# Optimization experiments

Hardware: AMD Instinct MI355X
Metric: run time of the kernel (lower is better)

## Reference

```python
import jax, jax.numpy as jnp
import numpy as np

EPS = 1e-5
NEIGHBOR_K = 3
NEG_SLOPE = 0.2

def _conv(x, w):
    # x: [N,C,H,W], w: [O,I,3,3], stride 1, SAME padding
    return jax.lax.conv_general_dilated(
        x, w, window_strides=(1, 1), padding='SAME',
        dimension_numbers=('NCHW', 'OIHW', 'NCHW'))

def _bn(x, gamma, beta):
    # BatchNorm2d in training mode: batch statistics over (N,H,W), biased var
    m = x.mean(axis=(0, 2, 3), keepdims=True)
    v = x.var(axis=(0, 2, 3), keepdims=True)
    xn = (x - m) * jax.lax.rsqrt(v + EPS)
    return xn * gamma.reshape(1, -1, 1, 1) + beta.reshape(1, -1, 1, 1)

def _lrelu(x):
    return jnp.where(x >= 0, x, NEG_SLOPE * x)

def _maxpool2(x):
    return jax.lax.reduce_window(x, -jnp.inf, jax.lax.max,
                                 (1, 1, 2, 2), (1, 1, 2, 2), 'VALID')

def _features(x, w1, g1, b1, w2, g2, b2, w3, g3, b3, w4, g4, b4):
    x = _maxpool2(_lrelu(_bn(_conv(x, w1), g1, b1)))
    x = _maxpool2(_lrelu(_bn(_conv(x, w2), g2, b2)))
    x = _lrelu(_bn(_conv(x, w3), g3, b3))
    x = _lrelu(_bn(_conv(x, w4), g4, b4))
    return x  # [N, 64, 21, 21]

def setup_inputs() -> dict:
    key = jax.random.key(0)
    ks = jax.random.split(key, 8)
    inp = {
        'input1': jax.random.normal(ks[0], (32, 3, 84, 84), jnp.float32),
        'input2': jax.random.normal(ks[1], (5, 5, 3, 84, 84), jnp.float32),
        'w1': jax.random.normal(ks[2], (64, 3, 3, 3), jnp.float32) * 0.1,
        'g1': jax.random.uniform(ks[3], (64,), jnp.float32, 0.5, 1.5),
        'b1': jnp.zeros((64,), jnp.float32),
        'w2': jax.random.normal(ks[4], (64, 64, 3, 3), jnp.float32) * 0.1,
        'g2': jax.random.uniform(ks[5], (64,), jnp.float32, 0.5, 1.5),
        'b2': jnp.zeros((64,), jnp.float32),
        'w3': jax.random.normal(ks[6], (64, 64, 3, 3), jnp.float32) * 0.1,
        'g3': jax.random.uniform(ks[7], (64,), jnp.float32, 0.5, 1.5),
        'b3': jnp.zeros((64,), jnp.float32),
        'w4': jax.random.normal(jax.random.fold_in(key, 100), (64, 64, 3, 3), jnp.float32) * 0.1,
        'g4': jax.random.uniform(jax.random.fold_in(key, 101), (64,), jnp.float32, 0.5, 1.5),
        'b4': jnp.zeros((64,), jnp.float32),
    }
    return inp

def reference(input1, input2, w1, g1, b1, w2, g2, b2, w3, g3, b3, w4, g4, b4):
    params = (w1, g1, b1, w2, g2, b2, w3, g3, b3, w4, g4, b4)
    # Query features: [B, C, h, w]
    q = _features(input1, *params)
    B, C, h, w = q.shape
    hw = h * w
    Q = q.reshape(B, C, hw).transpose(0, 2, 1)            # [B, hw, C]
    qn = jnp.linalg.norm(Q, axis=2, keepdims=True)        # [B, hw, 1]
    # Support features, BN stats per class-batch (matches per-class forward)
    s = jax.vmap(lambda x: _features(x, *params))(input2) # [nc, shot, C, h, w]
    nc, shot = s.shape[0], s.shape[1]
    S = s.transpose(0, 2, 1, 3, 4).reshape(nc, C, shot * hw)  # [nc, C, M]
    sn = jnp.linalg.norm(S, axis=1, keepdims=True)            # [nc, 1, M]
    # Cosine similarities: [B, nc, hw, M]
    sims = jnp.einsum('bqc,ncm->bnqm', Q, S)
    sims = sims / (qn[:, None, :, :] * sn[None, :, :, :])
    topv = jax.lax.top_k(sims, NEIGHBOR_K)[0]              # [B, nc, hw, k]
    return topv.sum(axis=(2, 3))                           # [B, nc]
```

## Files before the change

### kernel.cpp

```cpp
#include <hip/hip_runtime.h>
#include <hip/hip_bf16.h>
#include <stdint.h>

#define NQ 32
#define NCLS 5
#define SHOT 5
#define NIMG 57
#define P1 7056
#define P2 1764
#define P3 441
#define MM (SHOT*P3)
#define EPSB 1e-5f
#define SLOPE 0.2f
#define NEGINF -3.4e38f
#define NREP 32
#define QBLK 128
#define NQB 4

typedef __attribute__((ext_vector_type(8))) short short8;
typedef __attribute__((ext_vector_type(4))) float f32x4;

__device__ inline float ldf(const float* p) { return *p; }
__device__ inline float ldf(const __hip_bfloat16* p) { return __bfloat162float(*p); }

__device__ __forceinline__ unsigned short bf16bits(float v)
{
    __hip_bfloat16 h = __float2bfloat16(v);
    return *reinterpret_cast<unsigned short*>(&h);
}

__global__ void pack_all_k(const float* __restrict__ w1, const float* __restrict__ w2,
                           const float* __restrict__ w3, const float* __restrict__ w4,
                           unsigned short* __restrict__ wpk1, unsigned short* __restrict__ wpk2,
                           unsigned short* __restrict__ wpk3, unsigned short* __restrict__ wpk4)
{
    int i = blockIdx.x * 256 + threadIdx.x;
    if (i < 3 * 36864) {
        int set = i / 36864, ii = i - set * 36864;
        const float* w = (set == 0) ? w2 : (set == 1) ? w3 : w4;
        unsigned short* wpk = (set == 0) ? wpk2 : (set == 1) ? wpk3 : wpk4;
        int j = ii & 7, lane = (ii >> 3) & 63, chunk = ii >> 9;
        int nt = chunk & 3, half = (chunk >> 2) & 1, t = chunk >> 3;
        int co = nt * 16 + (lane & 15);
        int ci = half * 32 + (lane >> 4) * 8 + j;
        wpk[ii] = bf16bits(w[co * 576 + ci * 9 + t]);
    } else {
        int ii = i - 3 * 36864;
        if (ii >= 4096) return;
        int j = ii & 7, lane = (ii >> 3) & 63, c8 = ii >> 9;
        int nt = c8 & 3, f = c8 >> 2;
        int co = nt * 16 + (lane & 15), q = lane >> 4;
        int k = q * 8 + j;
        float val = 0.f;
        if (f == 0) {
            int t = k >> 2, ci = k & 3;
            if (ci < 3) val = w1[co * 27 + ci * 9 + t];
        } else if (k < 4) {
            int ci = k & 3;
            if (ci < 3) val = w1[co * 27 + ci * 9 + 8];
        }
        wpk1[ii] = bf16bits(val);
    }
}

__global__ __launch_bounds__(256) void conv1m_k(const float* __restrict__ in1,
                                                const float* __restrict__ in2,
                                                const unsigned short* __restrict__ wpk1,
                                                __hip_bfloat16* __restrict__ out,
                                                float* __restrict__ sums)
{
    constexpr int S = 84, P = P1, MBLK = 256, NB = 28, SPAN = MBLK + 2 * S + 2;
    __shared__ __align__(16) unsigned short ls4[SPAN * 4];
    __shared__ float qs[4][64], qs2[4][64];
    int img = blockIdx.x / NB;
    int p0 = (blockIdx.x % NB) * MBLK;
    int tid = threadIdx.x, lane = tid & 63, wv = tid >> 6;
    int col = lane & 15, quad = lane >> 4;
    const float* in = (img < NQ) ? in1 + (size_t)img * 3 * P1
                                 : in2 + (size_t)(img - NQ) * 3 * P1;
    for (int u = tid; u < SPAN; u += 256) {
        int p = p0 - S - 1 + u;
        union { unsigned short us[4]; uint2 u2; } o;
        o.u2 = (uint2){0u, 0u};
        if (p >= 0 && p < P) {
            o.us[0] = bf16bits(in[p]);
            o.us[1] = bf16bits(in[P1 + p]);
            o.us[2] = bf16bits(in[2 * P1 + p]);
        }
        *(uint2*)(ls4 + u * 4) = o.u2;
    }
    const short8* wb = (const short8*)wpk1;
    short8 b0[4], b1[4];
    #pragma unroll
    for (int nt = 0; nt < 4; ++nt) {
        b0[nt] = wb[(size_t)(nt * 64 + lane)];
        b1[nt] = wb[(size_t)((4 + nt) * 64 + lane)];
    }
    int t0 = 2 * quad, t1 = t0 + 1;
    int d0 = (t0 / 3 - 1) * S + (t0 % 3 - 1);
    int d1 = (t1 / 3 - 1) * S + (t1 % 3 - 1);
    const int d8 = S + 1;
    int tx0 = t0 % 3, tx1 = t1 % 3;
    __syncthreads();
    f32x4 acc[4][4];
    #pragma unroll
    for (int mt = 0; mt < 4; ++mt)
        #pragma unroll
        for (int nt = 0; nt < 4; ++nt) acc[mt][nt] = (f32x4){0.f, 0.f, 0.f, 0.f};
    #pragma unroll
    for (int mt = 0; mt < 4; ++mt) {
        int pl = wv * 64 + mt * 16 + col;
        int xm = (p0 + pl) % S;
        int base = pl + S + 1;
        uint2 h0 = *(const uint2*)(ls4 + (base + d0) * 4);
        uint2 h1 = *(const uint2*)(ls4 + (base + d1) * 4);
        uint2 h8 = *(const uint2*)(ls4 + (base + d8) * 4);
        bool ok0 = (tx0 == 0) ? (xm >= 1) : ((tx0 == 2) ? (xm <= S - 2) : true);
        bool ok1 = (tx1 == 0) ? (xm >= 1) : ((tx1 == 2) ? (xm <= S - 2) : true);
        bool ok8 = (quad == 0) && (xm <= S - 2);
        if (!ok0) h0 = (uint2){0u, 0u};
        if (!ok1) h1 = (uint2){0u, 0u};
        if (!ok8) h8 = (uint2){0u, 0u};
        union { uint4 u; short8 s; } ca, cb;
        ca.u = (uint4){h0.x, h0.y, h1.x, h1.y};
        cb.u = (uint4){h8.x, h8.y, 0u, 0u};
        #pragma unroll
        for (int nt = 0; nt < 4; ++nt) {
            acc[mt][nt] = __builtin_amdgcn_mfma_f32_16x16x32_bf16(ca.s, b0[nt], acc[mt][nt], 0, 0, 0);
            acc[mt][nt] = __builtin_amdgcn_mfma_f32_16x16x32_bf16(cb.s, b1[nt], acc[mt][nt], 0, 0, 0);
        }
    }
    float s[4] = {0.f, 0.f, 0.f, 0.f}, s2[4] = {0.f, 0.f, 0.f, 0.f};
    __hip_bfloat16* ob = out + (size_t)img * P * 64;
    #pragma unroll
    for (int mt = 0; mt < 4; ++mt) {
        int tb = p0 + wv * 64 + mt * 16 + quad * 4;
        #pragma unroll
        for (int reg = 0; reg < 4; ++reg) {
            int pr = tb + reg;
            if (pr < P) {
                #pragma unroll
                for (int nt = 0; nt < 4; ++nt) {
                    float v = acc[mt][nt][reg];
                    ob[(size_t)pr * 64 + nt * 16 + col] = __float2bfloat16(v);
                    s[nt] += v;
                    s2[nt] = fmaf(v, v, s2[nt]);
                }
            }
        }
    }
    #pragma unroll
    for (int d = 16; d < 64; d <<= 1)
        #pragma unroll
        for (int nt = 0; nt < 4; ++nt) {
            s[nt] += __shfl_xor(s[nt], d, 64);
            s2[nt] += __shfl_xor(s2[nt], d, 64);
        }
    if (quad == 0) {
        #pragma unroll
        for (int nt = 0; nt < 4; ++nt) {
            qs[wv][nt * 16 + col] = s[nt];
            qs2[wv][nt * 16 + col] = s2[nt];
        }
    }
    __syncthreads();
    if (wv == 0) {
        int g = (img < NQ) ? 0 : 1 + (img - NQ) / SHOT;
        int rep = blockIdx.x & (NREP - 1);
        float ts = qs[0][lane] + qs[1][lane] + qs[2][lane] + qs[3][lane];
        float ts2 = qs2[0][lane] + qs2[1][lane] + qs2[2][lane] + qs2[3][lane];
        float* base = sums + ((size_t)(g * 64 + lane) * 2) * NREP + rep;
        atomicAdd(base, ts);
        atomicAdd(base + NREP, ts2);
    }
}

template <int S, int MBLK>
__global__ __launch_bounds__(256) void conv64m_k(const unsigned short* __restrict__ in,
                                                 const unsigned short* __restrict__ wpk,
                                                 float* __restrict__ out,
                                                 float* __restrict__ sums)
{
    constexpr int P = S * S;
    constexpr int MT = MBLK / 64;
    constexpr int NB = (P + MBLK - 1) / MBLK;
    constexpr int SPAN = MBLK + 2 * S + 2;
    __shared__ __align__(16) unsigned short ls[SPAN * 72];
    __shared__ float qs[4][64], qs2[4][64];
    int img = blockIdx.x / NB;
    int p0 = (blockIdx.x % NB) * MBLK;
    int tid = threadIdx.x;
    int lane = tid & 63, wv = tid >> 6;
    int col = lane & 15, quad = lane >> 4;
    const unsigned short* ib = in + (size_t)img * P * 64;
    for (int u = tid; u < SPAN * 8; u += 256) {
        int pix = u >> 3, part = u & 7;
        int p = p0 - S - 1 + pix;
        short8 v = {0, 0, 0, 0, 0, 0, 0, 0};
        if (p >= 0 && p < P) v = *(const short8*)(ib + (size_t)p * 64 + part * 8);
        *(short8*)(ls + pix * 72 + part * 8) = v;
    }
    __syncthreads();
    f32x4 acc[MT][4];
    #pragma unroll
    for (int mt = 0; mt < MT; ++mt)
        #pragma unroll
        for (int nt = 0; nt < 4; ++nt) acc[mt][nt] = (f32x4){0.f, 0.f, 0.f, 0.f};
    bool mok0[MT], mok2[MT];
    #pragma unroll
    for (int mt = 0; mt < MT; ++mt) {
        int xm = (p0 + wv * (MT * 16) + mt * 16 + col) % S;
        mok0[mt] = xm >= 1;
        mok2[mt] = xm <= S - 2;
    }
    const short8* wb = (const short8*)wpk;
    #pragma unroll
    for (int ky = 0; ky < 3; ++ky) {
        #pragma unroll
        for (int kx = 0; kx < 3; ++kx) {
            int t = ky * 3 + kx;
            int d = (ky - 1) * S + (kx - 1);
            #pragma unroll
            for (int half = 0; half < 2; ++half) {
                short8 b[4];
                #pragma unroll
                for (int nt = 0; nt < 4; ++nt)
                    b[nt] = wb[((t * 2 + half) * 4 + nt) * 64 + lane];
                #pragma unroll
                for (int mt = 0; mt < MT; ++mt) {
                    int idx = wv * (MT * 16) + mt * 16 + col + S + 1 + d;
                    short8 a = *(const short8*)(ls + idx * 72 + half * 32 + quad * 8);
                    bool ok = (kx == 0) ? mok0[mt] : (kx == 2) ? mok2[mt] : true;
                    if (!ok) a = (short8){0, 0, 0, 0, 0, 0, 0, 0};
                    #pragma unroll
                    for (int nt = 0; nt < 4; ++nt)
                        acc[mt][nt] = __builtin_amdgcn_mfma_f32_16x16x32_bf16(a, b[nt], acc[mt][nt], 0, 0, 0);
                }
            }
        }
    }
    float s[4] = {0.f, 0.f, 0.f, 0.f}, s2[4] = {0.f, 0.f, 0.f, 0.f};
    float* ob = out + (size_t)img * P * 64;
    #pragma unroll
    for (int mt = 0; mt < MT; ++mt) {
        int tb = p0 + wv * (MT * 16) + mt * 16 + quad * 4;
        #pragma unroll
        for (int reg = 0; reg < 4; ++reg) {
            int pr = tb + reg;
            if (pr < P) {
                #pragma unroll
                for (int nt = 0; nt < 4; ++nt) {
                    float v = acc[mt][nt][reg];
                    ob[(size_t)pr * 64 + nt * 16 + col] = v;
                    s[nt] += v;
                    s2[nt] = fmaf(v, v, s2[nt]);
                }
            }
        }
    }
    #pragma unroll
    for (int d = 16; d < 64; d <<= 1)
        #pragma unroll
        for (int nt = 0; nt < 4; ++nt) {
            s[nt] += __shfl_xor(s[nt], d, 64);
            s2[nt] += __shfl_xor(s2[nt], d, 64);
        }
    if (quad == 0) {
        #pragma unroll
        for (int nt = 0; nt < 4; ++nt) {
            qs[wv][nt * 16 + col] = s[nt];
            qs2[wv][nt * 16 + col] = s2[nt];
        }
    }
    __syncthreads();
    if (wv == 0) {
        int g = (img < NQ) ? 0 : 1 + (img - NQ) / SHOT;
        int rep = blockIdx.x & (NREP - 1);
        float ts = qs[0][lane] + qs[1][lane] + qs[2][lane] + qs[3][lane];
        float ts2 = qs2[0][lane] + qs2[1][lane] + qs2[2][lane] + qs2[3][lane];
        float* base = sums + ((size_t)(g * 64 + lane) * 2) * NREP + rep;
        atomicAdd(base, ts);
        atomicAdd(base + NREP, ts2);
    }
}

__global__ void finalize_k(const float* __restrict__ sums, float* __restrict__ ms,
                           const float* __restrict__ gamma, const float* __restrict__ beta, int P)
{
    int i = blockIdx.x * blockDim.x + threadIdx.x;
    if (i >= 6 * 64) return;
    int g = i >> 6, c = i & 63;
    const float* ps = sums + (size_t)i * 2 * NREP;
    float s = 0.f, s2 = 0.f;
    #pragma unroll
    for (int r = 0; r < NREP; ++r) { s += ps[r]; s2 += ps[NREP + r]; }
    float cnt = (float)((g == 0 ? NQ : SHOT) * P);
    float mean = s / cnt;
    float var = s2 / cnt - mean * mean;
    float a = rsqrtf(var + EPSB) * gamma[c];
    ms[i * 2] = a;
    ms[i * 2 + 1] = fmaf(-mean, a, beta[c]);
}

template <typename T>
__global__ __launch_bounds__(256) void bnpool_k(const T* __restrict__ x, const float* __restrict__ ms,
                                                __hip_bfloat16* __restrict__ out, int Win)
{
    int Wout = Win >> 1, Pout = Wout * Wout;
    size_t idx = (size_t)blockIdx.x * 256 + threadIdx.x;
    size_t total = (size_t)NIMG * Pout * 64;
    if (idx >= total) return;
    int c = (int)(idx & 63);
    size_t t = idx >> 6;
    int p = (int)(t % Pout);
    int img = (int)(t / Pout);
    int y = p / Wout, xo = p - y * Wout;
    int g = (img < NQ) ? 0 : 1 + (img - NQ) / SHOT;
    float a = ms[(g * 64 + c) * 2], bb = ms[(g * 64 + c) * 2 + 1];
    const T* base = x + (((size_t)img * Win + 2 * y) * Win + 2 * xo) * 64 + c;
    float mx = -3.4e38f;
    #pragma unroll
    for (int dy = 0; dy < 2; ++dy)
        #pragma unroll
        for (int dx = 0; dx < 2; ++dx) {
            float v = ldf(base + ((size_t)dy * Win + dx) * 64);
            v = fmaf(v, a, bb);
            v = v >= 0.f ? v : SLOPE * v;
            mx = fmaxf(mx, v);
        }
    out[idx] = __float2bfloat16(mx);
}

__global__ __launch_bounds__(256) void bnact_k(const float* __restrict__ x, const float* __restrict__ ms,
                                               __hip_bfloat16* __restrict__ out)
{
    size_t idx = (size_t)blockIdx.x * 256 + threadIdx.x;
    size_t total = (size_t)NIMG * P3 * 64;
    if (idx >= total) return;
    int c = (int)(idx & 63);
    int img = (int)(idx >> 6) / P3;
    int g = (img < NQ) ? 0 : 1 + (img - NQ) / SHOT;
    float v = fmaf(x[idx], ms[(g * 64 + c) * 2], ms[(g * 64 + c) * 2 + 1]);
    out[idx] = __float2bfloat16(v >= 0.f ? v : SLOPE * v);
}

__global__ __launch_bounds__(256) void bnnorm_k(const float* __restrict__ x, const float* __restrict__ ms,
                                                __hip_bfloat16* __restrict__ out)
{
    int lane = threadIdx.x & 63, wvr = threadIdx.x >> 6;
    int pix = blockIdx.x * 4 + wvr;
    if (pix >= NIMG * P3) return;
    int img = pix / P3;
    int g = (img < NQ) ? 0 : 1 + (img - NQ) / SHOT;
    float v = fmaf(x[(size_t)pix * 64 + lane], ms[(g * 64 + lane) * 2], ms[(g * 64 + lane) * 2 + 1]);
    v = v >= 0.f ? v : SLOPE * v;
    float ss = v * v;
    #pragma unroll
    for (int d = 32; d > 0; d >>= 1) ss += __shfl_xor(ss, d, 64);
    out[(size_t)pix * 64 + lane] = __float2bfloat16(v * rsqrtf(ss));
}

__device__ __forceinline__ void ins3(float v, float& t0, float& t1, float& t2)
{
    float n1 = __builtin_amdgcn_fmed3f(v, t0, t1);
    float n2 = __builtin_amdgcn_fmed3f(v, t1, t2);
    t0 = fmaxf(t0, v);
    t1 = n1;
    t2 = n2;
}

__global__ __launch_bounds__(256) void sim_k(const __hip_bfloat16* __restrict__ fhat,
                                             float* __restrict__ out)
{
    __shared__ __align__(16) unsigned short sl[64 * 72];
    int t = blockIdx.x;
    int qb = t % NQB;
    int n = (t / NQB) % NCLS;
    int bq = t / (NQB * NCLS);
    int tid = threadIdx.x, lane = tid & 63, wv = tid >> 6;
    int col = lane & 15, quad = lane >> 4;
    short8 a0[2], a1[2];
    #pragma unroll
    for (int qt = 0; qt < 2; ++qt) {
        int q = qb * QBLK + wv * 32 + qt * 16 + col;
        int qc = q < P3 ? q : P3 - 1;
        const unsigned short* qp = (const unsigned short*)fhat + ((size_t)bq * P3 + qc) * 64;
        a0[qt] = *(const short8*)(qp + quad * 8);
        a1[qt] = *(const short8*)(qp + 32 + quad * 8);
    }
    const unsigned short* sp = (const unsigned short*)fhat + (size_t)(NQ + n * SHOT) * P3 * 64;
    float t0[2][4], t1[2][4], t2[2][4];
    #pragma unroll
    for (int qt = 0; qt < 2; ++qt)
        #pragma unroll
        for (int r = 0; r < 4; ++r) { t0[qt][r] = NEGINF; t1[qt][r] = NEGINF; t2[qt][r] = NEGINF; }
    for (int mc = 0; mc < 35; ++mc) {
        int m0 = mc * 64;
        __syncthreads();
        #pragma unroll
        for (int pass = 0; pass < 2; ++pass) {
            int row = (tid >> 3) + pass * 32;
            int cc = (tid & 7) * 8;
            int m = m0 + row;
            short8 vv = {0, 0, 0, 0, 0, 0, 0, 0};
            if (m < MM) vv = *(const short8*)(sp + (size_t)m * 64 + cc);
            *(short8*)(sl + row * 72 + cc) = vv;
        }
        __syncthreads();
        #pragma unroll
        for (int mt = 0; mt < 4; ++mt) {
            int mbase = m0 + mt * 16;
            if (mbase >= MM) continue;
            const unsigned short* sr = sl + (mt * 16 + col) * 72;
            short8 b0 = *(const short8*)(sr + quad * 8);
            short8 b1 = *(const short8*)(sr + 32 + quad * 8);
            if (mbase + 15 < MM) {
                #pragma unroll
                for (int qt = 0; qt < 2; ++qt) {
                    f32x4 acc = {0.f, 0.f, 0.f, 0.f};
                    acc = __builtin_amdgcn_mfma_f32_16x16x32_bf16(a0[qt], b0, acc, 0, 0, 0);
                    acc = __builtin_amdgcn_mfma_f32_16x16x32_bf16(a1[qt], b1, acc, 0, 0, 0);
                    #pragma unroll
                    for (int r = 0; r < 4; ++r) ins3(acc[r], t0[qt][r], t1[qt][r], t2[qt][r]);
                }
            } else {
                float bias = (mbase + col < MM) ? 0.f : NEGINF;
                #pragma unroll
                for (int qt = 0; qt < 2; ++qt) {
                    f32x4 acc = {0.f, 0.f, 0.f, 0.f};
                    acc = __builtin_amdgcn_mfma_f32_16x16x32_bf16(a0[qt], b0, acc, 0, 0, 0);
                    acc = __builtin_amdgcn_mfma_f32_16x16x32_bf16(a1[qt], b1, acc, 0, 0, 0);
                    #pragma unroll
                    for (int r = 0; r < 4; ++r) ins3(acc[r] + bias, t0[qt][r], t1[qt][r], t2[qt][r]);
                }
            }
        }
    }
    #pragma unroll
    for (int d = 1; d < 16; d <<= 1)
        #pragma unroll
        for (int qt = 0; qt < 2; ++qt)
            #pragma unroll
            for (int r = 0; r < 4; ++r) {
                float u0 = __shfl_xor(t0[qt][r], d, 64);
                float u1 = __shfl_xor(t1[qt][r], d, 64);
                float u2 = __shfl_xor(t2[qt][r], d, 64);
                ins3(u0, t0[qt][r], t1[qt][r], t2[qt][r]);
                ins3(u1, t0[qt][r], t1[qt][r], t2[qt][r]);
                ins3(u2, t0[qt][r], t1[qt][r], t2[qt][r]);
            }
    float s = 0.f;
    if (col == 0) {
        #pragma unroll
        for (int qt = 0; qt < 2; ++qt)
            #pragma unroll
            for (int r = 0; r < 4; ++r) {
                int q = qb * QBLK + wv * 32 + qt * 16 + quad * 4 + r;
                if (q < P3) s += t0[qt][r] + t1[qt][r] + t2[qt][r];
            }
    }
    #pragma unroll
    for (int d = 32; d > 0; d >>= 1) s += __shfl_xor(s, d, 64);
    if (lane == 0 && s != 0.f) atomicAdd(&out[bq * NCLS + n], s);
    if (lane == 0 && s == 0.f) atomicAdd(&out[bq * NCLS + n], 0.f);
}

extern "C" void kernel_launch(void* const* d_in, const int* in_sizes, int n_in,
                              void* d_out, int out_size, void* d_ws, size_t ws_size,
                              hipStream_t stream)
{
    const float* input1 = (const float*)d_in[0];
    const float* input2 = (const float*)d_in[1];
    const float* w1 = (const float*)d_in[2];
    const float* g1 = (const float*)d_in[3];
    const float* b1 = (const float*)d_in[4];
    const float* w2 = (const float*)d_in[5];
    const float* g2 = (const float*)d_in[6];
    const float* b2 = (const float*)d_in[7];
    const float* w3 = (const float*)d_in[8];
    const float* g3 = (const float*)d_in[9];
    const float* b3 = (const float*)d_in[10];
    const float* w4 = (const float*)d_in[11];
    const float* g4 = (const float*)d_in[12];
    const float* b4 = (const float*)d_in[13];
    float* out = (float*)d_out;

    char* w8 = (char*)d_ws;
    const size_t oB = 51480576;
    const size_t oT = oB + 12870144;
    const size_t STG = 6 * 64 * 2 * NREP * sizeof(float);
    __hip_bfloat16* conv1raw = (__hip_bfloat16*)(w8 + 0);
    float* conv2raw = (float*)(w8 + 0);
    float* conv3raw = (float*)(w8 + 0);
    __hip_bfloat16* act3 = (__hip_bfloat16*)(w8 + 6435072);
    float* conv4raw = (float*)(w8 + 9652608);
    __hip_bfloat16* fhat = (__hip_bfloat16*)(w8 + 16087680);
    __hip_bfloat16* pooled1 = (__hip_bfloat16*)(w8 + oB);
    __hip_bfloat16* pooled2 = (__hip_bfloat16*)(w8 + oB);
    float* sums = (float*)(w8 + oT);
    float* ms = (float*)(w8 + oT + 4 * STG);
    unsigned short* wpk2 = (unsigned short*)(w8 + oT + 4 * STG + 12288);
    unsigned short* wpk3 = (unsigned short*)(w8 + oT + 4 * STG + 12288 + 73728);
    unsigned short* wpk4 = (unsigned short*)(w8 + oT + 4 * STG + 12288 + 147456);
    unsigned short* wpk1 = (unsigned short*)(w8 + oT + 4 * STG + 12288 + 221184);
    if (ws_size < oT + 4 * STG + 12288 + 221184 + 8192) return;
    float* sums1 = sums;
    float* sums2 = sums + 6 * 64 * 2 * NREP;
    float* sums3 = sums2 + 6 * 64 * 2 * NREP;
    float* sums4 = sums3 + 6 * 64 * 2 * NREP;

    hipMemsetAsync(d_out, 0, (size_t)out_size * sizeof(float), stream);
    hipMemsetAsync(sums, 0, 4 * STG, stream);

    pack_all_k<<<448, 256, 0, stream>>>(w1, w2, w3, w4, wpk1, wpk2, wpk3, wpk4);

    conv1m_k<<<NIMG * 28, 256, 0, stream>>>(input1, input2, wpk1, conv1raw, sums1);
    finalize_k<<<2, 256, 0, stream>>>(sums1, ms + 0, g1, b1, P1);
    bnpool_k<__hip_bfloat16><<<25137, 256, 0, stream>>>(conv1raw, ms + 0, pooled1, 84);
    conv64m_k<42, 256><<<NIMG * 7, 256, 0, stream>>>((const unsigned short*)pooled1, wpk2, conv2raw, sums2);
    finalize_k<<<2, 256, 0, stream>>>(sums2, ms + 768, g2, b2, P2);
    bnpool_k<float><<<6285, 256, 0, stream>>>(conv2raw, ms + 768, pooled2, 42);
    conv64m_k<21, 128><<<NIMG * 4, 256, 0, stream>>>((const unsigned short*)pooled2, wpk3, conv3raw, sums3);
    finalize_k<<<2, 256, 0, stream>>>(sums3, ms + 1536, g3, b3, P3);
    bnact_k<<<6285, 256, 0, stream>>>(conv3raw, ms + 1536, act3);
    conv64m_k<21, 128><<<NIMG * 4, 256, 0, stream>>>((const unsigned short*)act3, wpk4, conv4raw, sums4);
    finalize_k<<<2, 256, 0, stream>>>(sums4, ms + 2304, g4, b4, P3);
    bnnorm_k<<<6285, 256, 0, stream>>>(conv4raw, ms + 2304, fhat);
    sim_k<<<NQ * NCLS * NQB, 256, 0, stream>>>(fhat, out);
}
```

Baseline: 261.4 us.

## Split similarity top-k across support ranges with merge kernel; store conv2 output as bf16

The similarity kernel now splits each (query, class) pair's support dimension into four ranges and uses smaller 64-query tiles. This raises the block count from 640 to 4480 for better GPU occupancy. Each block writes partial top-3 lists to workspace, and a new merge kernel combines them and writes the outputs directly, which removes the output memset and the atomics. Separately, the conv2 raw output is stored as bf16 instead of fp32 to halve its write and read traffic, at some cost in precision before the batch norm.

```diff
diff --git a/kernel.cpp b/kernel.cpp
--- a/kernel.cpp
+++ b/kernel.cpp
@@ -14,14 +14,16 @@
 #define SLOPE 0.2f
 #define NEGINF -3.4e38f
 #define NREP 32
-#define QBLK 128
-#define NQB 4
+#define MSPAN 576
+#define MRNG 4
 
 typedef __attribute__((ext_vector_type(8))) short short8;
 typedef __attribute__((ext_vector_type(4))) float f32x4;
 
 __device__ inline float ldf(const float* p) { return *p; }
 __device__ inline float ldf(const __hip_bfloat16* p) { return __bfloat162float(*p); }
+__device__ inline void stf(float* p, float v) { *p = v; }
+__device__ inline void stf(__hip_bfloat16* p, float v) { *p = __float2bfloat16(v); }
 
 __device__ __forceinline__ unsigned short bf16bits(float v)
 {
@@ -175,10 +177,10 @@
     }
 }
 
-template <int S, int MBLK>
+template <int S, int MBLK, typename OT>
 __global__ __launch_bounds__(256) void conv64m_k(const unsigned short* __restrict__ in,
                                                  const unsigned short* __restrict__ wpk,
-                                                 float* __restrict__ out,
+                                                 OT* __restrict__ out,
                                                  float* __restrict__ sums)
 {
     constexpr int P = S * S;
@@ -240,7 +242,7 @@
         }
     }
     float s[4] = {0.f, 0.f, 0.f, 0.f}, s2[4] = {0.f, 0.f, 0.f, 0.f};
-    float* ob = out + (size_t)img * P * 64;
+    OT* ob = out + (size_t)img * P * 64;
     #pragma unroll
     for (int mt = 0; mt < MT; ++mt) {
         int tb = p0 + wv * (MT * 16) + mt * 16 + quad * 4;
@@ -251,7 +253,7 @@
                 #pragma unroll
                 for (int nt = 0; nt < 4; ++nt) {
                     float v = acc[mt][nt][reg];
-                    ob[(size_t)pr * 64 + nt * 16 + col] = v;
+                    stf(ob + (size_t)pr * 64 + nt * 16 + col, v);
                     s[nt] += v;
                     s2[nt] = fmaf(v, v, s2[nt]);
                 }
@@ -369,33 +371,31 @@
     t2 = n2;
 }
 
-__global__ __launch_bounds__(256) void sim_k(const __hip_bfloat16* __restrict__ fhat,
-                                             float* __restrict__ out)
+__global__ __launch_bounds__(256) void sim_part_k(const __hip_bfloat16* __restrict__ fhat,
+                                                  float* __restrict__ part)
 {
     __shared__ __align__(16) unsigned short sl[64 * 72];
     int t = blockIdx.x;
-    int qb = t % NQB;
-    int n = (t / NQB) % NCLS;
-    int bq = t / (NQB * NCLS);
+    int mr = t & 3;
+    int qb = (t >> 2) % 7;
+    int n = (t / 28) % NCLS;
+    int bq = t / (28 * NCLS);
     int tid = threadIdx.x, lane = tid & 63, wv = tid >> 6;
     int col = lane & 15, quad = lane >> 4;
-    short8 a0[2], a1[2];
-    #pragma unroll
-    for (int qt = 0; qt < 2; ++qt) {
-        int q = qb * QBLK + wv * 32 + qt * 16 + col;
-        int qc = q < P3 ? q : P3 - 1;
-        const unsigned short* qp = (const unsigned short*)fhat + ((size_t)bq * P3 + qc) * 64;
-        a0[qt] = *(const short8*)(qp + quad * 8);
-        a1[qt] = *(const short8*)(qp + 32 + quad * 8);
-    }
+    int q = qb * 64 + wv * 16 + col;
+    int qc = q < P3 ? q : P3 - 1;
+    const unsigned short* qp = (const unsigned short*)fhat + ((size_t)bq * P3 + qc) * 64;
+    short8 a0 = *(const short8*)(qp + quad * 8);
+    short8 a1 = *(const short8*)(qp + 32 + quad * 8);
     const unsigned short* sp = (const unsigned short*)fhat + (size_t)(NQ + n * SHOT) * P3 * 64;
-    float t0[2][4], t1[2][4], t2[2][4];
-    #pragma unroll
-    for (int qt = 0; qt < 2; ++qt)
-        #pragma unroll
-        for (int r = 0; r < 4; ++r) { t0[qt][r] = NEGINF; t1[qt][r] = NEGINF; t2[qt][r] = NEGINF; }
-    for (int mc = 0; mc < 35; ++mc) {
-        int m0 = mc * 64;
+    int m_lo = mr * MSPAN;
+    int m_cnt = MM - m_lo; if (m_cnt > MSPAN) m_cnt = MSPAN;
+    int nch = (m_cnt + 63) >> 6;
+    float t0[4], t1[4], t2[4];
+    #pragma unroll
+    for (int r = 0; r < 4; ++r) { t0[r] = NEGINF; t1[r] = NEGINF; t2[r] = NEGINF; }
+    for (int c = 0; c < nch; ++c) {
+        int m0 = m_lo + c * 64;
         __syncthreads();
         #pragma unroll
         for (int pass = 0; pass < 2; ++pass) {
@@ -414,55 +414,67 @@
             const unsigned short* sr = sl + (mt * 16 + col) * 72;
             short8 b0 = *(const short8*)(sr + quad * 8);
             short8 b1 = *(const short8*)(sr + 32 + quad * 8);
+            f32x4 acc = {0.f, 0.f, 0.f, 0.f};
+            acc = __builtin_amdgcn_mfma_f32_16x16x32_bf16(a0, b0, acc, 0, 0, 0);
+            acc = __builtin_amdgcn_mfma_f32_16x16x32_bf16(a1, b1, acc, 0, 0, 0);
             if (mbase + 15 < MM) {
                 #pragma unroll
-                for (int qt = 0; qt < 2; ++qt) {
-                    f32x4 acc = {0.f, 0.f, 0.f, 0.f};
-                    acc = __builtin_amdgcn_mfma_f32_16x16x32_bf16(a0[qt], b0, acc, 0, 0, 0);
-                    acc = __builtin_amdgcn_mfma_f32_16x16x32_bf16(a1[qt], b1, acc, 0, 0, 0);
-                    #pragma unroll
-                    for (int r = 0; r < 4; ++r) ins3(acc[r], t0[qt][r], t1[qt][r], t2[qt][r]);
-                }
+                for (int r = 0; r < 4; ++r) ins3(acc[r], t0[r], t1[r], t2[r]);
             } else {
                 float bias = (mbase + col < MM) ? 0.f : NEGINF;
                 #pragma unroll
-                for (int qt = 0; qt < 2; ++qt) {
-                    f32x4 acc = {0.f, 0.f, 0.f, 0.f};
-                    acc = __builtin_amdgcn_mfma_f32_16x16x32_bf16(a0[qt], b0, acc, 0, 0, 0);
-                    acc = __builtin_amdgcn_mfma_f32_16x16x32_bf16(a1[qt], b1, acc, 0, 0, 0);
-                    #pragma unroll
-                    for (int r = 0; r < 4; ++r) ins3(acc[r] + bias, t0[qt][r], t1[qt][r], t2[qt][r]);
-                }
+                for (int r = 0; r < 4; ++r) ins3(acc[r] + bias, t0[r], t1[r], t2[r]);
             }
         }
     }
     #pragma unroll
     for (int d = 1; d < 16; d <<= 1)
         #pragma unroll
-        for (int qt = 0; qt < 2; ++qt)
-            #pragma unroll
-            for (int r = 0; r < 4; ++r) {
-                float u0 = __shfl_xor(t0[qt][r], d, 64);
-                float u1 = __shfl_xor(t1[qt][r], d, 64);
-                float u2 = __shfl_xor(t2[qt][r], d, 64);
-                ins3(u0, t0[qt][r], t1[qt][r], t2[qt][r]);
-                ins3(u1, t0[qt][r], t1[qt][r], t2[qt][r]);
-                ins3(u2, t0[qt][r], t1[qt][r], t2[qt][r]);
-            }
+        for (int r = 0; r < 4; ++r) {
+            float u0 = __shfl_xor(t0[r], d, 64);
+            float u1 = __shfl_xor(t1[r], d, 64);
+            float u2 = __shfl_xor(t2[r], d, 64);
+            ins3(u0, t0[r], t1[r], t2[r]);
+            ins3(u1, t0[r], t1[r], t2[r]);
+            ins3(u2, t0[r], t1[r], t2[r]);
+        }
+    if (col == 0) {
+        #pragma unroll
+        for (int r = 0; r < 4; ++r) {
+            int ql = wv * 16 + quad * 4 + r;
+            float* pp = part + ((((size_t)(bq * NCLS + n) * 7 + qb) * 4 + mr) * 64 + ql) * 3;
+            pp[0] = t0[r];
+            pp[1] = t1[r];
+            pp[2] = t2[r];
+        }
+    }
+}
+
+__global__ __launch_bounds__(256) void sim_merge_k(const float* __restrict__ part,
+                                                   float* __restrict__ out)
+{
+    __shared__ float red[4];
+    int b = blockIdx.x;
+    int tid = threadIdx.x, lane = tid & 63, wv = tid >> 6;
     float s = 0.f;
-    if (col == 0) {
-        #pragma unroll
-        for (int qt = 0; qt < 2; ++qt)
-            #pragma unroll
-            for (int r = 0; r < 4; ++r) {
-                int q = qb * QBLK + wv * 32 + qt * 16 + quad * 4 + r;
-                if (q < P3) s += t0[qt][r] + t1[qt][r] + t2[qt][r];
-            }
+    for (int q = tid; q < P3; q += 256) {
+        int qb = q >> 6, ql = q & 63;
+        const float* pp = part + (((size_t)b * 7 + qb) * 4 * 64 + ql) * 3;
+        float v0 = pp[0], v1 = pp[1], v2 = pp[2];
+        #pragma unroll
+        for (int mr = 1; mr < 4; ++mr) {
+            const float* pm = pp + (size_t)mr * 192;
+            ins3(pm[0], v0, v1, v2);
+            ins3(pm[1], v0, v1, v2);
+            ins3(pm[2], v0, v1, v2);
+        }
+        s += v0 + v1 + v2;
     }
     #pragma unroll
     for (int d = 32; d > 0; d >>= 1) s += __shfl_xor(s, d, 64);
-    if (lane == 0 && s != 0.f) atomicAdd(&out[bq * NCLS + n], s);
-    if (lane == 0 && s == 0.f) atomicAdd(&out[bq * NCLS + n], 0.f);
+    if (lane == 0) red[wv] = s;
+    __syncthreads();
+    if (tid == 0) out[b] = red[0] + red[1] + red[2] + red[3];
 }
 
 extern "C" void kernel_launch(void* const* d_in, const int* in_sizes, int n_in,
@@ -490,7 +502,7 @@
     const size_t oT = oB + 12870144;
     const size_t STG = 6 * 64 * 2 * NREP * sizeof(float);
     __hip_bfloat16* conv1raw = (__hip_bfloat16*)(w8 + 0);
-    float* conv2raw = (float*)(w8 + 0);
+    __hip_bfloat16* conv2raw = (__hip_bfloat16*)(w8 + 0);
     float* conv3raw = (float*)(w8 + 0);
     __hip_bfloat16* act3 = (__hip_bfloat16*)(w8 + 6435072);
     float* conv4raw = (float*)(w8 + 9652608);
@@ -503,13 +515,14 @@
     unsigned short* wpk3 = (unsigned short*)(w8 + oT + 4 * STG + 12288 + 73728);
     unsigned short* wpk4 = (unsigned short*)(w8 + oT + 4 * STG + 12288 + 147456);
     unsigned short* wpk1 = (unsigned short*)(w8 + oT + 4 * STG + 12288 + 221184);
-    if (ws_size < oT + 4 * STG + 12288 + 221184 + 8192) return;
+    const size_t oP = oT + 4 * STG + 12288 + 221184 + 8192;
+    float* part = (float*)(w8 + oP);
+    if (ws_size < oP + (size_t)NQ * NCLS * 7 * 4 * 64 * 3 * sizeof(float)) return;
     float* sums1 = sums;
     float* sums2 = sums + 6 * 64 * 2 * NREP;
     float* sums3 = sums2 + 6 * 64 * 2 * NREP;
     float* sums4 = sums3 + 6 * 64 * 2 * NREP;
 
-    hipMemsetAsync(d_out, 0, (size_t)out_size * sizeof(float), stream);
     hipMemsetAsync(sums, 0, 4 * STG, stream);
 
     pack_all_k<<<448, 256, 0, stream>>>(w1, w2, w3, w4, wpk1, wpk2, wpk3, wpk4);
@@ -517,14 +530,18 @@
     conv1m_k<<<NIMG * 28, 256, 0, stream>>>(input1, input2, wpk1, conv1raw, sums1);
     finalize_k<<<2, 256, 0, stream>>>(sums1, ms + 0, g1, b1, P1);
     bnpool_k<__hip_bfloat16><<<25137, 256, 0, stream>>>(conv1raw, ms + 0, pooled1, 84);
-    conv64m_k<42, 256><<<NIMG * 7, 256, 0, stream>>>((const unsigned short*)pooled1, wpk2, conv2raw, sums2);
+    conv64m_k<42, 256, __hip_bfloat16><<<NIMG * 7, 256, 0, stream>>>(
+        (const unsigned short*)pooled1, wpk2, conv2raw, sums2);
     finalize_k<<<2, 256, 0, stream>>>(sums2, ms + 768, g2, b2, P2);
-    bnpool_k<float><<<6285, 256, 0, stream>>>(conv2raw, ms + 768, pooled2, 42);
-    conv64m_k<21, 128><<<NIMG * 4, 256, 0, stream>>>((const unsigned short*)pooled2, wpk3, conv3raw, sums3);
+    bnpool_k<__hip_bfloat16><<<6285, 256, 0, stream>>>(conv2raw, ms + 768, pooled2, 42);
+    conv64m_k<21, 128, float><<<NIMG * 4, 256, 0, stream>>>(
+        (const unsigned short*)pooled2, wpk3, conv3raw, sums3);
     finalize_k<<<2, 256, 0, stream>>>(sums3, ms + 1536, g3, b3, P3);
     bnact_k<<<6285, 256, 0, stream>>>(conv3raw, ms + 1536, act3);
-    conv64m_k<21, 128><<<NIMG * 4, 256, 0, stream>>>((const unsigned short*)act3, wpk4, conv4raw, sums4);
+    conv64m_k<21, 128, float><<<NIMG * 4, 256, 0, stream>>>(
+        (const unsigned short*)act3, wpk4, conv4raw, sums4);
     finalize_k<<<2, 256, 0, stream>>>(sums4, ms + 2304, g4, b4, P3);
     bnnorm_k<<<6285, 256, 0, stream>>>(conv4raw, ms + 2304, fhat);
-    sim_k<<<NQ * NCLS * NQB, 256, 0, stream>>>(fhat, out);
-}
+    sim_part_k<<<NQ * NCLS * 7 * MRNG, 256, 0, stream>>>(fhat, part);
+    sim_merge_k<<<NQ * NCLS, 256, 0, stream>>>(part, out);
+}
```

New measurement: 256.8 us. No clear change (-1.7%).
